# Kernel tuning notes

Measured on AMD Instinct MI355X. Metric: run time of the kernel, lower is better.

The kernel has to match this reference:

```python
import jax, jax.numpy as jnp
import numpy as np

EPS = 1e-5

def conv_block(x, w, b, a, g, bt):
    # x: [B,Cin,T,F]; w: [Cout,Cin]; b: [Cout]; a: scalar PReLU slope; g,bt: [Cout,F]
    y = jnp.einsum('bctf,oc->botf', x, w) + b[None, :, None, None]
    y = jnp.maximum(y, 0.0) + a * jnp.minimum(y, 0.0)  # PReLU (single shared slope)
    mu = jnp.mean(y, axis=(1, 3), keepdims=True)
    var = jnp.var(y, axis=(1, 3), keepdims=True)       # unbiased=False
    y = (y - mu) / jnp.sqrt(var + EPS)
    return y * g[None, :, None, :] + bt[None, :, None, :]

# vmap over heads: weights have leading head axis, x is shared
_head_block = jax.vmap(conv_block, in_axes=(None, 0, 0, 0, 0, 0))


def setup_inputs() -> dict:
    key = jax.random.key(0)
    B, C, T, F = 8, 64, 1024, 64
    H, HID = 4, 4
    DV = C // H
    ks = jax.random.split(key, 16)
    s = 1.0 / np.sqrt(C)
    inp = {
        'x': jax.random.normal(ks[0], (B, C, T, F), jnp.float32),
        # per-head Q conv blocks
        'qw': jax.random.normal(ks[1], (H, HID, C), jnp.float32) * s,
        'qb': jax.random.normal(ks[2], (H, HID), jnp.float32) * 0.01,
        'qa': jnp.full((H,), 0.25, jnp.float32),
        'qg': jnp.ones((H, HID, F), jnp.float32),
        'qbeta': jnp.zeros((H, HID, F), jnp.float32),
        # per-head K conv blocks
        'kw': jax.random.normal(ks[3], (H, HID, C), jnp.float32) * s,
        'kb': jax.random.normal(ks[4], (H, HID), jnp.float32) * 0.01,
        'ka': jnp.full((H,), 0.25, jnp.float32),
        'kg': jnp.ones((H, HID, F), jnp.float32),
        'kbeta': jnp.zeros((H, HID, F), jnp.float32),
        # per-head V conv blocks (out = C//H)
        'vw': jax.random.normal(ks[5], (H, DV, C), jnp.float32) * s,
        'vb': jax.random.normal(ks[6], (H, DV), jnp.float32) * 0.01,
        'va': jnp.full((H,), 0.25, jnp.float32),
        'vg': jnp.ones((H, DV, F), jnp.float32),
        'vbeta': jnp.zeros((H, DV, F), jnp.float32),
        # final 'likear' conv block
        'lw': jax.random.normal(ks[7], (C, C), jnp.float32) * s,
        'lb': jax.random.normal(ks[8], (C,), jnp.float32) * 0.01,
        'la': jnp.float32(0.25),
        'lg': jnp.ones((C, F), jnp.float32),
        'lbeta': jnp.zeros((C, F), jnp.float32),
    }
    return inp


def reference(x, qw, qb, qa, qg, qbeta, kw, kb, ka, kg, kbeta,
              vw, vb, va, vg, vbeta, lw, lb, la, lg, lbeta):
    B, C, T, F = x.shape
    H = qw.shape[0]
    HID = qw.shape[1]
    DV = C // H
    embed = H * F  # embed_size = num_heads * num_freqs

    Q = _head_block(x, qw, qb, qa, qg, qbeta)  # [H,B,HID,T,F]
    K = _head_block(x, kw, kb, ka, kg, kbeta)  # [H,B,HID,T,F]
    V = _head_block(x, vw, vb, va, vg, vbeta)  # [H,B,DV,T,F]

    # cat over dim 0 == head-major reshape; transpose(1,2)+flatten(2)
    Ql = Q.reshape(H * B, HID, T, F).transpose(0, 2, 1, 3).reshape(H * B, T, HID * F)
    Kl = K.reshape(H * B, HID, T, F).transpose(0, 2, 1, 3).reshape(H * B, T, HID * F)
    Vl = V.reshape(H * B, DV, T, F).transpose(0, 2, 1, 3).reshape(H * B, T, DV * F)

    scores = jnp.einsum('ntd,nsd->nts', Ql, Kl) / jnp.sqrt(jnp.float32(embed))
    attn = jax.nn.softmax(scores, axis=-1)               # [HB,T,T]
    A = jnp.einsum('nts,nsd->ntd', attn, Vl)             # [HB,T,DV*F]

    A = A.reshape(H * B, T, DV, F).transpose(0, 2, 1, 3)  # [HB,DV,T,F]
    A = A.reshape(H, B, DV, T, F).transpose(1, 0, 2, 3, 4).reshape(B, C, T, F)

    out = conv_block(A, lw, lb, la, lg, lbeta)
    return out + x
```

## Files before the change

### kernel.cpp

```cpp
#include <hip/hip_runtime.h>

typedef unsigned short u16;
typedef __attribute__((ext_vector_type(8))) short short8;
typedef __attribute__((ext_vector_type(4))) float f32x4;

#define EPSV 1e-5f

__device__ __forceinline__ u16 f2bf(float f) {
    unsigned u = __float_as_uint(f);
    u += 0x7fffu + ((u >> 16) & 1u);
    return (u16)(u >> 16);
}

__device__ __forceinline__ f32x4 mfma_bf16(short8 a, short8 b, f32x4 c) {
    return __builtin_amdgcn_mfma_f32_16x16x32_bf16(a, b, c, 0, 0, 0);
}

__device__ __forceinline__ void gload_lds16(const void* g, void* l) {
    __builtin_amdgcn_global_load_lds((const __attribute__((address_space(1))) void*)g,
                                     (__attribute__((address_space(3))) void*)l, 16, 0, 0);
}

__global__ __launch_bounds__(256) void k_qkv(
    const float* __restrict__ x,
    const float* __restrict__ qw, const float* __restrict__ qb, const float* __restrict__ qa,
    const float* __restrict__ qg, const float* __restrict__ qbt,
    const float* __restrict__ kw, const float* __restrict__ kb, const float* __restrict__ ka,
    const float* __restrict__ kg, const float* __restrict__ kbt,
    const float* __restrict__ vw, const float* __restrict__ vb, const float* __restrict__ va,
    const float* __restrict__ vg, const float* __restrict__ vbt,
    u16* __restrict__ Qb, u16* __restrict__ Kb, u16* __restrict__ Vb)
{
    __shared__ u16 xT[64][72];
    __shared__ u16 wsb[96][72];
    __shared__ float ys[96][64];
    __shared__ float bias_s[96], slope_s[96];

    const int tid = threadIdx.x, w = tid >> 6, lane = tid & 63;
    const int b = blockIdx.x >> 10, t = blockIdx.x & 1023;

#pragma unroll
    for (int i = 0; i < 24; i++) {
        int idx = tid + i * 256;
        int row = idx >> 6, c = idx & 63;
        float wv = (row < 16) ? qw[idx] : ((row < 32) ? kw[idx - 1024] : vw[idx - 2048]);
        wsb[row][c] = f2bf(wv);
    }
    if (tid < 96) {
        int row = tid; float bv, sv;
        if (row < 16)      { bv = qb[row];      sv = qa[row >> 2]; }
        else if (row < 32) { bv = kb[row - 16]; sv = ka[(row - 16) >> 2]; }
        else               { bv = vb[row - 32]; sv = va[(row - 32) >> 4]; }
        bias_s[row] = bv; slope_s[row] = sv;
    }
    const float* xbt = x + ((size_t)(b * 64) * 1024 + t) * 64;
#pragma unroll
    for (int k = 0; k < 4; k++) {
        int chunk = tid + k * 256;
        int c = chunk >> 4, q = chunk & 15;
        float4 v = *(const float4*)(xbt + (size_t)c * 65536 + q * 4);
        xT[q * 4 + 0][c] = f2bf(v.x);
        xT[q * 4 + 1][c] = f2bf(v.y);
        xT[q * 4 + 2][c] = f2bf(v.z);
        xT[q * 4 + 3][c] = f2bf(v.w);
    }
    __syncthreads();

#pragma unroll
    for (int i = 0; i < 6; i++) {
        int tile = w * 6 + i;
        int mt = tile >> 2, nt = tile & 3;
        f32x4 acc = {0.f, 0.f, 0.f, 0.f};
#pragma unroll
        for (int kt = 0; kt < 2; kt++) {
            short8 a  = *(const short8*)(&wsb[mt * 16 + (lane & 15)][kt * 32 + (lane >> 4) * 8]);
            short8 bf = *(const short8*)(&xT [nt * 16 + (lane & 15)][kt * 32 + (lane >> 4) * 8]);
            acc = mfma_bf16(a, bf, acc);
        }
        int colf = nt * 16 + (lane & 15);
#pragma unroll
        for (int j = 0; j < 4; j++) {
            int row = mt * 16 + (lane >> 4) * 4 + j;
            float y = acc[j] + bias_s[row];
            float sl = slope_s[row];
            y = (y > 0.f) ? y : sl * y;
            ys[row][colf] = y;
        }
    }
    __syncthreads();

    const int h = w;
    {
        float v0[4]; float s = 0.f, ss = 0.f;
#pragma unroll
        for (int o = 0; o < 4; o++) { float y = ys[h * 4 + o][lane]; v0[o] = y; s += y; ss += y * y; }
#pragma unroll
        for (int m = 1; m < 64; m <<= 1) { s += __shfl_xor(s, m, 64); ss += __shfl_xor(ss, m, 64); }
        float mu = s * (1.f / 256.f), var = ss * (1.f / 256.f) - mu * mu;
        float rs = rsqrtf(var + EPSV);
        size_t base = ((size_t)(h * 8 + b) * 1024 + t) * 256;
#pragma unroll
        for (int o = 0; o < 4; o++) {
            float val = (v0[o] - mu) * rs * qg[(h * 4 + o) * 64 + lane] + qbt[(h * 4 + o) * 64 + lane];
            Qb[base + o * 64 + lane] = f2bf(val);
        }
    }
    {
        float v0[4]; float s = 0.f, ss = 0.f;
#pragma unroll
        for (int o = 0; o < 4; o++) { float y = ys[16 + h * 4 + o][lane]; v0[o] = y; s += y; ss += y * y; }
#pragma unroll
        for (int m = 1; m < 64; m <<= 1) { s += __shfl_xor(s, m, 64); ss += __shfl_xor(ss, m, 64); }
        float mu = s * (1.f / 256.f), var = ss * (1.f / 256.f) - mu * mu;
        float rs = rsqrtf(var + EPSV);
        size_t base = ((size_t)(h * 8 + b) * 1024 + t) * 256;
#pragma unroll
        for (int o = 0; o < 4; o++) {
            float val = (v0[o] - mu) * rs * kg[(h * 4 + o) * 64 + lane] + kbt[(h * 4 + o) * 64 + lane];
            Kb[base + o * 64 + lane] = f2bf(val);
        }
    }
    {
        float v0[16]; float s = 0.f, ss = 0.f;
#pragma unroll
        for (int o = 0; o < 16; o++) { float y = ys[32 + h * 16 + o][lane]; v0[o] = y; s += y; ss += y * y; }
#pragma unroll
        for (int m = 1; m < 64; m <<= 1) { s += __shfl_xor(s, m, 64); ss += __shfl_xor(ss, m, 64); }
        float mu = s * (1.f / 1024.f), var = ss * (1.f / 1024.f) - mu * mu;
        float rs = rsqrtf(var + EPSV);
        size_t base = ((size_t)(h * 8 + b) * 1024 + t) * 1024;
#pragma unroll
        for (int o = 0; o < 16; o++) {
            float val = (v0[o] - mu) * rs * vg[(h * 16 + o) * 64 + lane] + vbt[(h * 16 + o) * 64 + lane];
            Vb[base + o * 64 + lane] = f2bf(val);
        }
    }
}

__global__ __launch_bounds__(256) void k_vtrans(const u16* __restrict__ Vb, u16* __restrict__ Vt)
{
    __shared__ u16 ts[64][72];
    const int tid = threadIdx.x;
    const int idx = blockIdx.x;
    const int n = idx >> 8, rest = idx & 255;
    const int s0 = (rest >> 4) * 64, d0 = (rest & 15) * 64;
    const size_t nb = (size_t)n << 20;

#pragma unroll
    for (int i = 0; i < 2; i++) {
        int chunk = tid + i * 256;
        int row = chunk >> 3, q = chunk & 7;
        uint4 v = *(const uint4*)(Vb + nb + (size_t)(s0 + row) * 1024 + d0 + q * 8);
        *(uint4*)(&ts[row][q * 8]) = v;
    }
    __syncthreads();
#pragma unroll
    for (int i = 0; i < 2; i++) {
        int chunk = tid + i * 256;
        int orow = chunk >> 3, q = chunk & 7;
        uint4 o;
        o.x = (unsigned)ts[q * 8 + 0][orow] | ((unsigned)ts[q * 8 + 1][orow] << 16);
        o.y = (unsigned)ts[q * 8 + 2][orow] | ((unsigned)ts[q * 8 + 3][orow] << 16);
        o.z = (unsigned)ts[q * 8 + 4][orow] | ((unsigned)ts[q * 8 + 5][orow] << 16);
        o.w = (unsigned)ts[q * 8 + 6][orow] | ((unsigned)ts[q * 8 + 7][orow] << 16);
        *(uint4*)(Vt + nb + (size_t)(d0 + orow) * 1024 + s0 + q * 8) = o;
    }
}

__global__ __launch_bounds__(256) void k_attn(const u16* __restrict__ Qb, const u16* __restrict__ Kb,
                                              u16* __restrict__ P)
{
    __shared__ u16 Ks[4][16 * 256];
    __shared__ float red[2][4][16];

    const int bid = blockIdx.x;
    const int n = (bid & 7) + ((bid >> 9) << 3);
    const int qt = (bid >> 3) & 63;
    const int q0 = qt * 16;
    const int tid = threadIdx.x, w = tid >> 6, lane = tid & 63;
    const int grp = lane >> 4, lc = lane & 15;

    const u16* Qn = Qb + ((size_t)n << 18);
    const u16* Kn = Kb + ((size_t)n << 18);

    short8 qf[8];
#pragma unroll
    for (int kt = 0; kt < 8; kt++)
        qf[kt] = *(const short8*)(Qn + (size_t)(q0 + lc) * 256 + kt * 32 + grp * 8);

    u16* KsW = Ks[w];
    const int l_row = lane >> 5;
    const int l_cs = (lane & 31) * 8;

    f32x4 sacc[16];
#pragma unroll
    for (int st = 0; st < 16; st++) {
        int s0 = w * 256 + st * 16;
#pragma unroll
        for (int c = 0; c < 8; c++) {
            int row = c * 2 + l_row;
            int col = l_cs ^ ((row & 7) << 3);
            gload_lds16(Kn + (size_t)(s0 + row) * 256 + col, KsW + c * 512);
        }
        __syncthreads();
        f32x4 a = {0.f, 0.f, 0.f, 0.f};
#pragma unroll
        for (int kt = 0; kt < 8; kt++) {
            int off = lc * 256 + ((kt * 32 + grp * 8) ^ ((lc & 7) << 3));
            short8 kf = *(const short8*)(KsW + off);
            a = mfma_bf16(qf[kt], kf, a);
        }
        sacc[st] = a;
        __syncthreads();
    }

    float mx[4] = {-1e30f, -1e30f, -1e30f, -1e30f};
#pragma unroll
    for (int st = 0; st < 16; st++)
#pragma unroll
        for (int j = 0; j < 4; j++) {
            float v = sacc[st][j] * 0.0625f;
            sacc[st][j] = v;
            mx[j] = fmaxf(mx[j], v);
        }
#pragma unroll
    for (int m = 1; m < 16; m <<= 1)
#pragma unroll
        for (int j = 0; j < 4; j++) mx[j] = fmaxf(mx[j], __shfl_xor(mx[j], m, 64));

    if (lc == 0) {
#pragma unroll
        for (int j = 0; j < 4; j++) red[0][w][grp * 4 + j] = mx[j];
    }
    __syncthreads();
    float gm[4], sm[4] = {0.f, 0.f, 0.f, 0.f};
#pragma unroll
    for (int j = 0; j < 4; j++) {
        int row = grp * 4 + j;
        gm[j] = fmaxf(fmaxf(red[0][0][row], red[0][1][row]), fmaxf(red[0][2][row], red[0][3][row]));
    }
#pragma unroll
    for (int st = 0; st < 16; st++)
#pragma unroll
        for (int j = 0; j < 4; j++) {
            float p = __expf(sacc[st][j] - gm[j]);
            sacc[st][j] = p;
            sm[j] += p;
        }
#pragma unroll
    for (int m = 1; m < 16; m <<= 1)
#pragma unroll
        for (int j = 0; j < 4; j++) sm[j] += __shfl_xor(sm[j], m, 64);
    if (lc == 0) {
#pragma unroll
        for (int j = 0; j < 4; j++) red[1][w][grp * 4 + j] = sm[j];
    }
    __syncthreads();

    u16* Pn = P + ((size_t)n << 20);
    float inv[4];
#pragma unroll
    for (int j = 0; j < 4; j++) {
        int row = grp * 4 + j;
        float tot = red[1][0][row] + red[1][1][row] + red[1][2][row] + red[1][3][row];
        inv[j] = 1.f / tot;
    }
#pragma unroll
    for (int st = 0; st < 16; st++)
#pragma unroll
        for (int j = 0; j < 4; j++) {
            Pn[(size_t)(q0 + grp * 4 + j) * 1024 + w * 256 + st * 16 + lc] = f2bf(sacc[st][j] * inv[j]);
        }
}

__global__ __launch_bounds__(256) void k_pv(const u16* __restrict__ P, const u16* __restrict__ Vt,
                                            float* __restrict__ out)
{
    const int bid = blockIdx.x;
    const int n = (bid & 7) + ((bid >> 9) << 3);
    const int tile = (bid >> 3) & 63;
    const int tm = tile >> 3, tn = tile & 7;
    const int tid = threadIdx.x, w = tid >> 6, lane = tid & 63;
    const int wr = w >> 1, wc = w & 1;
    const int lc = lane & 15, grp = lane >> 4;

    __shared__ u16 As[128 * 32];
    __shared__ u16 Bs[128 * 32];

    const u16* Pa = P  + ((size_t)n << 20) + (size_t)tm * 128 * 1024;
    const u16* Va = Vt + ((size_t)n << 20) + (size_t)tn * 128 * 1024;

    f32x4 acc[4][4];
#pragma unroll
    for (int mi = 0; mi < 4; mi++)
#pragma unroll
        for (int ni = 0; ni < 4; ni++) acc[mi][ni] = (f32x4){0.f, 0.f, 0.f, 0.f};

    for (int ks = 0; ks < 32; ks++) {
        int k0 = ks * 32;
#pragma unroll
        for (int jj = 0; jj < 2; jj++) {
            int seg = jj * 4 + w;
            int chunk = seg * 64 + lane;
            int row = chunk >> 2, q = chunk & 3;
            gload_lds16(Pa + (size_t)row * 1024 + k0 + q * 8, As + seg * 512);
            gload_lds16(Va + (size_t)row * 1024 + k0 + q * 8, Bs + seg * 512);
        }
        __syncthreads();
        short8 af[4], bfr[4];
#pragma unroll
        for (int mi = 0; mi < 4; mi++)
            af[mi] = *(const short8*)(As + (wr * 64 + mi * 16 + lc) * 32 + grp * 8);
#pragma unroll
        for (int ni = 0; ni < 4; ni++)
            bfr[ni] = *(const short8*)(Bs + (wc * 64 + ni * 16 + lc) * 32 + grp * 8);
#pragma unroll
        for (int mi = 0; mi < 4; mi++)
#pragma unroll
            for (int ni = 0; ni < 4; ni++)
                acc[mi][ni] = mfma_bf16(af[mi], bfr[ni], acc[mi][ni]);
        __syncthreads();
    }

    const int h = n >> 3, b = n & 7;
#pragma unroll
    for (int mi = 0; mi < 4; mi++)
#pragma unroll
        for (int ni = 0; ni < 4; ni++) {
            int d = tn * 128 + wc * 64 + ni * 16 + lc;
            int c = h * 16 + (d >> 6), f = d & 63;
#pragma unroll
            for (int j = 0; j < 4; j++) {
                int trow = tm * 128 + wr * 64 + mi * 16 + grp * 4 + j;
                out[(((size_t)b * 64 + c) * 1024 + trow) * 64 + f] = acc[mi][ni][j];
            }
        }
}

__global__ __launch_bounds__(256) void k_final(
    const float* __restrict__ Ain, const float* __restrict__ x,
    const float* __restrict__ lw, const float* __restrict__ lbias, const float* __restrict__ la,
    const float* __restrict__ lg, const float* __restrict__ lbt, float* __restrict__ out)
{
    __shared__ u16 AT[64][72];
    __shared__ u16 lwb[64][72];
    __shared__ float ys[64][64];
    __shared__ float red[8];

    const int tid = threadIdx.x, w = tid >> 6, lane = tid & 63;
    const int b = blockIdx.x >> 10, t = blockIdx.x & 1023;
    const int lc = lane & 15, grp = lane >> 4;

#pragma unroll
    for (int i = 0; i < 16; i++) {
        int idx = tid + i * 256;
        lwb[idx >> 6][idx & 63] = f2bf(lw[idx]);
    }
    const float* Abt = Ain + ((size_t)(b * 64) * 1024 + t) * 64;
#pragma unroll
    for (int k = 0; k < 4; k++) {
        int chunk = tid + k * 256;
        int c = chunk >> 4, q = chunk & 15;
        float4 v = *(const float4*)(Abt + (size_t)c * 65536 + q * 4);
        AT[q * 4 + 0][c] = f2bf(v.x);
        AT[q * 4 + 1][c] = f2bf(v.y);
        AT[q * 4 + 2][c] = f2bf(v.z);
        AT[q * 4 + 3][c] = f2bf(v.w);
    }
    __syncthreads();

    const float slope = la[0];
    float psum = 0.f, psq = 0.f;
#pragma unroll
    for (int nt = 0; nt < 4; nt++) {
        f32x4 acc = {0.f, 0.f, 0.f, 0.f};
#pragma unroll
        for (int kt = 0; kt < 2; kt++) {
            short8 a  = *(const short8*)(&lwb[w * 16 + lc][kt * 32 + grp * 8]);
            short8 bf = *(const short8*)(&AT [nt * 16 + lc][kt * 32 + grp * 8]);
            acc = mfma_bf16(a, bf, acc);
        }
#pragma unroll
        for (int j = 0; j < 4; j++) {
            int row = w * 16 + grp * 4 + j;
            float y = acc[j] + lbias[row];
            y = (y > 0.f) ? y : slope * y;
            ys[row][nt * 16 + lc] = y;
            psum += y; psq += y * y;
        }
    }
#pragma unroll
    for (int m = 1; m < 64; m <<= 1) { psum += __shfl_xor(psum, m, 64); psq += __shfl_xor(psq, m, 64); }
    if (lane == 0) { red[w] = psum; red[4 + w] = psq; }
    __syncthreads();
    float S  = red[0] + red[1] + red[2] + red[3];
    float SS = red[4] + red[5] + red[6] + red[7];
    float mu = S * (1.f / 4096.f), var = SS * (1.f / 4096.f) - mu * mu;
    float rs = rsqrtf(var + EPSV);

    for (int idx = tid; idx < 4096; idx += 256) {
        int o = idx >> 6, f = idx & 63;
        size_t gi = ((size_t)(b * 64 + o) * 1024 + t) * 64 + f;
        out[gi] = (ys[o][f] - mu) * rs * lg[idx] + lbt[idx] + x[gi];
    }
}

extern "C" void kernel_launch(void* const* d_in, const int* in_sizes, int n_in,
                              void* d_out, int out_size, void* d_ws, size_t ws_size,
                              hipStream_t stream)
{
    const float* x    = (const float*)d_in[0];
    const float* qw   = (const float*)d_in[1];
    const float* qb   = (const float*)d_in[2];
    const float* qa   = (const float*)d_in[3];
    const float* qg   = (const float*)d_in[4];
    const float* qbt  = (const float*)d_in[5];
    const float* kw   = (const float*)d_in[6];
    const float* kb   = (const float*)d_in[7];
    const float* ka   = (const float*)d_in[8];
    const float* kg   = (const float*)d_in[9];
    const float* kbt  = (const float*)d_in[10];
    const float* vw   = (const float*)d_in[11];
    const float* vb   = (const float*)d_in[12];
    const float* va   = (const float*)d_in[13];
    const float* vg   = (const float*)d_in[14];
    const float* vbt  = (const float*)d_in[15];
    const float* lw   = (const float*)d_in[16];
    const float* lb   = (const float*)d_in[17];
    const float* la   = (const float*)d_in[18];
    const float* lg   = (const float*)d_in[19];
    const float* lbt  = (const float*)d_in[20];

    float* out = (float*)d_out;

    u16* Vb = (u16*)d_ws;
    u16* Vt = (u16*)((char*)d_ws + ((size_t)64 << 20));
    u16* P  = Vb;
    u16* Qb = (u16*)d_out;
    u16* Kb = (u16*)((char*)d_out + ((size_t)16 << 20));

    k_qkv<<<dim3(8192), dim3(256), 0, stream>>>(x, qw, qb, qa, qg, qbt,
                                                kw, kb, ka, kg, kbt,
                                                vw, vb, va, vg, vbt, Qb, Kb, Vb);
    k_vtrans<<<dim3(8192), dim3(256), 0, stream>>>(Vb, Vt);
    k_attn<<<dim3(2048), dim3(256), 0, stream>>>(Qb, Kb, P);
    k_pv<<<dim3(2048), dim3(256), 0, stream>>>(P, Vt, out);
    k_final<<<dim3(8192), dim3(256), 0, stream>>>(out, x, lw, lb, la, lg, lbt, out);
}
```

Measured before the change: 370.7 us.

## Enlarge PV GEMM tiles to 256x256 with double-buffered LDS and swizzle

Rewrites the P·V kernel to use 512-thread blocks computing 256x256 output tiles instead of 128x128. Global-to-LDS loads are double-buffered so the next k-slice loads while the current one feeds MFMA. An XOR swizzle is applied to LDS column chunks to avoid bank conflicts, and MFMA issue priority is raised. This increases data reuse and overlaps memory with compute, at the cost of higher register use (32 accumulators per wave) and fewer blocks (512) for occupancy.

```diff
diff --git a/kernel.cpp b/kernel.cpp
--- a/kernel.cpp
+++ b/kernel.cpp
@@ -273,65 +273,83 @@
         }
 }
 
-__global__ __launch_bounds__(256) void k_pv(const u16* __restrict__ P, const u16* __restrict__ Vt,
-                                            float* __restrict__ out)
-{
+__global__ __launch_bounds__(512, 2) void k_pv(const u16* __restrict__ P, const u16* __restrict__ Vt,
+                                               float* __restrict__ out)
+{
+    __shared__ u16 lds[2][4][128 * 32];
+
     const int bid = blockIdx.x;
-    const int n = (bid & 7) + ((bid >> 9) << 3);
-    const int tile = (bid >> 3) & 63;
-    const int tm = tile >> 3, tn = tile & 7;
+    const int n = (bid & 7) + ((bid >> 7) << 3);
+    const int tile = (bid >> 3) & 15;
+    const int tm = tile >> 2, tn = tile & 3;
     const int tid = threadIdx.x, w = tid >> 6, lane = tid & 63;
-    const int wr = w >> 1, wc = w & 1;
+    const int wr = w >> 2, wc = w & 3;
     const int lc = lane & 15, grp = lane >> 4;
 
-    __shared__ u16 As[128 * 32];
-    __shared__ u16 Bs[128 * 32];
-
-    const u16* Pa = P  + ((size_t)n << 20) + (size_t)tm * 128 * 1024;
-    const u16* Va = Vt + ((size_t)n << 20) + (size_t)tn * 128 * 1024;
-
-    f32x4 acc[4][4];
-#pragma unroll
-    for (int mi = 0; mi < 4; mi++)
+    const u16* Pa = P  + ((size_t)n << 20) + (size_t)tm * 256 * 1024;
+    const u16* Va = Vt + ((size_t)n << 20) + (size_t)tn * 256 * 1024;
+
+    const int srow = tid >> 2, scc = tid & 3;
+    const int scol = (scc ^ (srow & 3)) * 8;
+    const int ldst = w * 512;
+
+    f32x4 acc[8][4];
+#pragma unroll
+    for (int mi = 0; mi < 8; mi++)
 #pragma unroll
         for (int ni = 0; ni < 4; ni++) acc[mi][ni] = (f32x4){0.f, 0.f, 0.f, 0.f};
 
+#define STAGE_PV(ks_, pb_)                                                        \
+    {                                                                             \
+        size_t k0_ = (size_t)(ks_) * 32;                                          \
+        gload_lds16(Pa + (size_t)srow * 1024 + k0_ + scol,         &lds[pb_][0][ldst]); \
+        gload_lds16(Pa + (size_t)(128 + srow) * 1024 + k0_ + scol, &lds[pb_][1][ldst]); \
+        gload_lds16(Va + (size_t)srow * 1024 + k0_ + scol,         &lds[pb_][2][ldst]); \
+        gload_lds16(Va + (size_t)(128 + srow) * 1024 + k0_ + scol, &lds[pb_][3][ldst]); \
+    }
+
+    STAGE_PV(0, 0);
+    __syncthreads();
+
+    const int rxor = (lc & 3);
     for (int ks = 0; ks < 32; ks++) {
-        int k0 = ks * 32;
-#pragma unroll
-        for (int jj = 0; jj < 2; jj++) {
-            int seg = jj * 4 + w;
-            int chunk = seg * 64 + lane;
-            int row = chunk >> 2, q = chunk & 3;
-            gload_lds16(Pa + (size_t)row * 1024 + k0 + q * 8, As + seg * 512);
-            gload_lds16(Va + (size_t)row * 1024 + k0 + q * 8, Bs + seg * 512);
-        }
+        int cur = ks & 1;
+        if (ks < 31) STAGE_PV(ks + 1, cur ^ 1);
+
+        const u16* As = lds[cur][wr];
+        const u16* Bs = lds[cur][2 + (wc >> 1)];
+        const int brow0 = (wc & 1) * 64;
+
+        short8 af[8], bf[4];
+#pragma unroll
+        for (int mi = 0; mi < 8; mi++)
+            af[mi] = *(const short8*)(As + (mi * 16 + lc) * 32 + ((grp ^ rxor) * 8));
+#pragma unroll
+        for (int ni = 0; ni < 4; ni++)
+            bf[ni] = *(const short8*)(Bs + (brow0 + ni * 16 + lc) * 32 + ((grp ^ rxor) * 8));
+
+        __builtin_amdgcn_s_setprio(1);
+#pragma unroll
+        for (int mi = 0; mi < 8; mi++)
+#pragma unroll
+            for (int ni = 0; ni < 4; ni++)
+                acc[mi][ni] = mfma_bf16(af[mi], bf[ni], acc[mi][ni]);
+        __builtin_amdgcn_s_setprio(0);
+
         __syncthreads();
-        short8 af[4], bfr[4];
-#pragma unroll
-        for (int mi = 0; mi < 4; mi++)
-            af[mi] = *(const short8*)(As + (wr * 64 + mi * 16 + lc) * 32 + grp * 8);
-#pragma unroll
-        for (int ni = 0; ni < 4; ni++)
-            bfr[ni] = *(const short8*)(Bs + (wc * 64 + ni * 16 + lc) * 32 + grp * 8);
-#pragma unroll
-        for (int mi = 0; mi < 4; mi++)
-#pragma unroll
-            for (int ni = 0; ni < 4; ni++)
-                acc[mi][ni] = mfma_bf16(af[mi], bfr[ni], acc[mi][ni]);
-        __syncthreads();
-    }
+    }
+#undef STAGE_PV
 
     const int h = n >> 3, b = n & 7;
 #pragma unroll
-    for (int mi = 0; mi < 4; mi++)
+    for (int mi = 0; mi < 8; mi++)
 #pragma unroll
         for (int ni = 0; ni < 4; ni++) {
-            int d = tn * 128 + wc * 64 + ni * 16 + lc;
+            int d = tn * 256 + wc * 64 + ni * 16 + lc;
             int c = h * 16 + (d >> 6), f = d & 63;
 #pragma unroll
             for (int j = 0; j < 4; j++) {
-                int trow = tm * 128 + wr * 64 + mi * 16 + grp * 4 + j;
+                int trow = tm * 256 + wr * 128 + mi * 16 + grp * 4 + j;
                 out[(((size_t)b * 64 + c) * 1024 + trow) * 64 + f] = acc[mi][ni][j];
             }
         }
@@ -444,6 +462,6 @@
                                                 vw, vb, va, vg, vbt, Qb, Kb, Vb);
     k_vtrans<<<dim3(8192), dim3(256), 0, stream>>>(Vb, Vt);
     k_attn<<<dim3(2048), dim3(256), 0, stream>>>(Qb, Kb, P);
-    k_pv<<<dim3(2048), dim3(256), 0, stream>>>(P, Vt, out);
+    k_pv<<<dim3(512), dim3(512), 0, stream>>>(P, Vt, out);
     k_final<<<dim3(8192), dim3(256), 0, stream>>>(out, x, lw, lb, la, lg, lbt, out);
 }
```

Result: faster. 337.6 us (-8.9%).
